# Kernel tuning notes

Hardware: AMD Instinct MI355X
Metric: run time of the kernel (lower is better)

## Reference

```python
import jax, jax.numpy as jnp
import numpy as np

KERNEL_SIZE = 37  # int((6*20-7)//3) = 37, already odd
PAD = (KERNEL_SIZE - 1) // 2  # 18


def moving_avg(x):
    """Edge-replicated moving average along token axis. x: [B, T, C]."""
    front = jnp.repeat(x[:, :1, :], PAD, axis=1)
    end = jnp.repeat(x[:, -1:, :], PAD, axis=1)
    xp = jnp.concatenate([front, x, end], axis=1)  # [B, T+2*PAD, C]
    cs = jnp.cumsum(xp, axis=1)
    cs = jnp.concatenate([jnp.zeros_like(cs[:, :1, :]), cs], axis=1)
    # window sums: length (T+2*PAD+1) - KERNEL_SIZE = T
    return (cs[:, KERNEL_SIZE:, :] - cs[:, :-KERNEL_SIZE, :]) / KERNEL_SIZE


def setup_inputs() -> dict:
    key = jax.random.key(0)
    ks = jax.random.split(key, 5)
    B, T, Cin, Cout = 4096, 17, 512, 512
    scale = 1.0 / np.sqrt(Cin)
    x = jax.random.normal(ks[0], (B, T, Cin), dtype=jnp.float32)
    W_seasonal = jax.random.uniform(ks[1], (T, Cout, Cin), jnp.float32, -scale, scale)
    b_seasonal = jax.random.uniform(ks[2], (T, Cout), jnp.float32, -scale, scale)
    W_trend = jax.random.uniform(ks[3], (T, Cout, Cin), jnp.float32, -scale, scale)
    b_trend = jax.random.uniform(ks[4], (T, Cout), jnp.float32, -scale, scale)
    return {"x": x, "W_seasonal": W_seasonal, "b_seasonal": b_seasonal,
            "W_trend": W_trend, "b_trend": b_trend}


def reference(x, W_seasonal, b_seasonal, W_trend, b_trend):
    trend = moving_avg(x)            # [B, T, Cin]
    seasonal = x - trend             # [B, T, Cin]
    # per-token (grouped) linear layers as one batched einsum
    s_out = jnp.einsum('btc,tdc->btd', seasonal, W_seasonal) + b_seasonal[None]
    t_out = jnp.einsum('btc,tdc->btd', trend, W_trend) + b_trend[None]
    return s_out + t_out
```

## Files before the change

kernel.cpp:

```cpp
#include <hip/hip_runtime.h>
#include <stdint.h>

#define B_N 4096
#define T_N 17
#define C_N 512

typedef __bf16 bf16x8 __attribute__((ext_vector_type(8)));
typedef float  f32x4  __attribute__((ext_vector_type(4)));

__device__ __forceinline__ unsigned short f2b(float f){
  unsigned u = __float_as_uint(f);
  return (unsigned short)((u + 0x7fffu + ((u >> 16) & 1u)) >> 16);
}
__device__ __forceinline__ unsigned pk2(float a, float b){
  return (unsigned)f2b(a) | ((unsigned)f2b(b) << 16);
}
__device__ __forceinline__ float blo(unsigned w){ return __uint_as_float(w << 16); }
__device__ __forceinline__ float bhi(unsigned w){ return __uint_as_float(w & 0xffff0000u); }

__device__ __forceinline__ void gll16(const void* g, void* l){
  __builtin_amdgcn_global_load_lds(
      (const __attribute__((address_space(1))) unsigned int*)g,
      (__attribute__((address_space(3))) unsigned int*)l, 16, 0, 0);
}

__global__ __launch_bounds__(256) void prep_w(
    const float* __restrict__ Ws, const float* __restrict__ Wt,
    unsigned short* __restrict__ wsb, unsigned short* __restrict__ dwb)
{
  const size_t i8 = ((size_t)blockIdx.x * 256 + threadIdx.x) * 8;
  float4 a0 = *(const float4*)(Ws + i8);
  float4 a1 = *(const float4*)(Ws + i8 + 4);
  float4 b0 = *(const float4*)(Wt + i8);
  float4 b1 = *(const float4*)(Wt + i8 + 4);
  uint4 oa, od;
  oa.x = pk2(a0.x, a0.y); oa.y = pk2(a0.z, a0.w);
  oa.z = pk2(a1.x, a1.y); oa.w = pk2(a1.z, a1.w);
  od.x = pk2(b0.x - a0.x, b0.y - a0.y); od.y = pk2(b0.z - a0.z, b0.w - a0.w);
  od.z = pk2(b1.x - a1.x, b1.y - a1.y); od.w = pk2(b1.z - a1.z, b1.w - a1.w);
  *(uint4*)(wsb + i8) = oa;
  *(uint4*)(dwb + i8) = od;
}

__global__ __launch_bounds__(256) void prep_bsum(
    const float* __restrict__ bs, const float* __restrict__ bt, float* __restrict__ o)
{
  const int i = blockIdx.x * 256 + threadIdx.x;
  o[i] = bs[i] + bt[i];
}

template<bool MAT>
__global__ __launch_bounds__(256) void prep_x(
    const float* __restrict__ x,
    unsigned short* __restrict__ o1,
    unsigned short* __restrict__ o2)
{
  const int idx = blockIdx.x * 256 + threadIdx.x;
  const int b = idx >> 6;
  const int c = (idx & 63) << 3;
  const float* xp = x + (size_t)b * (T_N * C_N) + c;
  float s[8] = {0,0,0,0,0,0,0,0};
  float f0[8], fl[8];
#pragma unroll
  for (int tt = 0; tt < T_N; ++tt){
    float4 w0 = *(const float4*)(xp + (size_t)tt * C_N);
    float4 w1 = *(const float4*)(xp + (size_t)tt * C_N + 4);
    float f[8] = {w0.x, w0.y, w0.z, w0.w, w1.x, w1.y, w1.z, w1.w};
    if (MAT){
      uint4 o;
      o.x = pk2(f[0],f[1]); o.y = pk2(f[2],f[3]);
      o.z = pk2(f[4],f[5]); o.w = pk2(f[6],f[7]);
      *(uint4*)(o1 + (size_t)b * (T_N*C_N) + (size_t)tt * C_N + c) = o;
    }
    if (tt == 0){
#pragma unroll
      for (int i=0;i<8;++i) f0[i] = f[i];
    }
    if (tt == T_N-1){
#pragma unroll
      for (int i=0;i<8;++i) fl[i] = f[i];
    }
#pragma unroll
    for (int i=0;i<8;++i) s[i] += f[i];
  }
  const float inv = 1.0f / 37.0f;
  float uu[8], vv[8];
#pragma unroll
  for (int i=0;i<8;++i){
    uu[i] = (s[i] + 18.0f * f0[i] + 2.0f * fl[i]) * inv;
    vv[i] = (fl[i] - f0[i]) * inv;
  }
  if (MAT){
#pragma unroll
    for (int tt = 0; tt < T_N; ++tt){
      const float tfv = (float)tt;
      float tr[8];
#pragma unroll
      for (int i=0;i<8;++i) tr[i] = fmaf(tfv, vv[i], uu[i]);
      uint4 o;
      o.x = pk2(tr[0],tr[1]); o.y = pk2(tr[2],tr[3]);
      o.z = pk2(tr[4],tr[5]); o.w = pk2(tr[6],tr[7]);
      *(uint4*)(o2 + (size_t)b * (T_N*C_N) + (size_t)tt * C_N + c) = o;
    }
  } else {
    uint4 ou, ov;
    ou.x = pk2(uu[0],uu[1]); ou.y = pk2(uu[2],uu[3]);
    ou.z = pk2(uu[4],uu[5]); ou.w = pk2(uu[6],uu[7]);
    ov.x = pk2(vv[0],vv[1]); ov.y = pk2(vv[2],vv[3]);
    ov.z = pk2(vv[4],vv[5]); ov.w = pk2(vv[6],vv[7]);
    *(uint4*)(o1 + (size_t)b * C_N + c) = ou;
    *(uint4*)(o2 + (size_t)b * C_N + c) = ov;
  }
}

template<bool MAT>
__global__ __launch_bounds__(256) void gemm_k(
    const float* __restrict__ x,
    const unsigned short* __restrict__ xb,
    const unsigned short* __restrict__ wsb,
    const unsigned short* __restrict__ dwb,
    const unsigned short* __restrict__ p1,
    const unsigned short* __restrict__ p2,
    const float* __restrict__ bsum,
    float* __restrict__ out)
{
  __shared__ alignas(16) unsigned short As[128*32];
  __shared__ alignas(16) unsigned short Bs[128*32];

  const int tid  = threadIdx.x;
  const int bx   = blockIdx.x;
  const int nt   = bx & 3;
  const int mt   = (bx >> 2) & 31;
  const int t    = bx >> 7;
  const int m0   = mt << 7;
  const int n0   = nt << 7;
  const int lane = tid & 63;
  const int wave = tid >> 6;
  const int wm   = (wave >> 1) << 6;
  const int wn   = (wave & 1) << 6;
  const int lr   = lane & 15;
  const int lj   = lane >> 4;
  const int swz  = (lr >> 1) & 3;

  f32x4 acc[4][4];
#pragma unroll
  for (int i=0;i<4;++i)
#pragma unroll
    for (int j=0;j<4;++j){ f32x4 z = {0.f,0.f,0.f,0.f}; acc[i][j] = z; }

  const float tf = (float)t;

  for (int kk = 0; kk < 32; ++kk){
    const int k0 = kk << 5;
    __syncthreads();
    if (MAT){
#pragma unroll
      for (int r = 0; r < 2; ++r){
        const int chunk = r*256 + tid;
        const int row = chunk >> 2;
        const int cgl = (chunk & 3) ^ ((row >> 1) & 3);
        const unsigned short* g = (k0 < 512)
          ? xb + ((size_t)(m0+row)*T_N + t)*C_N + k0 + cgl*8
          : p1 + ((size_t)(m0+row)*T_N + t)*C_N + (k0 - 512) + cgl*8;
        gll16(g, &As[chunk*8]);
      }
    } else if (k0 < 512){
#pragma unroll
      for (int r = 0; r < 2; ++r){
        const int chunk = r*256 + tid;
        const int row = chunk >> 2;
        const int cgl = (chunk & 3) ^ ((row >> 1) & 3);
        const float* g = x + ((size_t)(m0+row)*T_N + t)*C_N + k0 + cgl*8;
        float4 w0 = *(const float4*)g;
        float4 w1 = *(const float4*)(g + 4);
        uint4 o;
        o.x = pk2(w0.x, w0.y); o.y = pk2(w0.z, w0.w);
        o.z = pk2(w1.x, w1.y); o.w = pk2(w1.z, w1.w);
        *(uint4*)&As[chunk*8] = o;
      }
    } else {
#pragma unroll
      for (int r = 0; r < 2; ++r){
        const int chunk = r*256 + tid;
        const int row = chunk >> 2;
        const int cgl = (chunk & 3) ^ ((row >> 1) & 3);
        const size_t go = (size_t)(m0+row)*C_N + (k0 - 512) + cgl*8;
        uint4 uu = *(const uint4*)(p1 + go);
        uint4 vv = *(const uint4*)(p2 + go);
        uint4 o;
        o.x = pk2(fmaf(tf, blo(vv.x), blo(uu.x)), fmaf(tf, bhi(vv.x), bhi(uu.x)));
        o.y = pk2(fmaf(tf, blo(vv.y), blo(uu.y)), fmaf(tf, bhi(vv.y), bhi(uu.y)));
        o.z = pk2(fmaf(tf, blo(vv.z), blo(uu.z)), fmaf(tf, bhi(vv.z), bhi(uu.z)));
        o.w = pk2(fmaf(tf, blo(vv.w), blo(uu.w)), fmaf(tf, bhi(vv.w), bhi(uu.w)));
        *(uint4*)&As[chunk*8] = o;
      }
    }
#pragma unroll
    for (int r = 0; r < 2; ++r){
      const int chunk = r*256 + tid;
      const int row = chunk >> 2;
      const int cgl = (chunk & 3) ^ ((row >> 1) & 3);
      const unsigned short* g = (k0 < 512)
        ? wsb + ((size_t)t*C_N + n0 + row)*C_N + k0 + cgl*8
        : dwb + ((size_t)t*C_N + n0 + row)*C_N + (k0 - 512) + cgl*8;
      gll16(g, &Bs[chunk*8]);
    }
    __syncthreads();

    bf16x8 af[4], bf[4];
#pragma unroll
    for (int i=0;i<4;++i){
      const int row = wm + i*16 + lr;
      af[i] = *(const bf16x8*)&As[row*32 + ((lj ^ swz) * 8)];
    }
#pragma unroll
    for (int i=0;i<4;++i){
      const int row = wn + i*16 + lr;
      bf[i] = *(const bf16x8*)&Bs[row*32 + ((lj ^ swz) * 8)];
    }
#pragma unroll
    for (int mi=0;mi<4;++mi)
#pragma unroll
      for (int ni=0;ni<4;++ni)
        acc[mi][ni] = __builtin_amdgcn_mfma_f32_16x16x32_bf16(af[mi], bf[ni], acc[mi][ni], 0, 0, 0);
  }

  float bias[4];
#pragma unroll
  for (int ni=0;ni<4;++ni)
    bias[ni] = bsum[(size_t)t*C_N + n0 + wn + ni*16 + lr];

#pragma unroll
  for (int mi=0;mi<4;++mi){
#pragma unroll
    for (int r=0;r<4;++r){
      const int m = m0 + wm + mi*16 + lj*4 + r;
      float* op = out + ((size_t)m*T_N + t)*C_N + n0 + wn + lr;
#pragma unroll
      for (int ni=0;ni<4;++ni)
        op[ni*16] = acc[mi][ni][r] + bias[ni];
    }
  }
}

extern "C" void kernel_launch(void* const* d_in, const int* in_sizes, int n_in,
                              void* d_out, int out_size, void* d_ws, size_t ws_size,
                              hipStream_t stream)
{
  const float* x   = (const float*)d_in[0];
  const float* Wsl = (const float*)d_in[1];
  const float* bsl = (const float*)d_in[2];
  const float* Wtr = (const float*)d_in[3];
  const float* btr = (const float*)d_in[4];
  float* out = (float*)d_out;

  const size_t WSB_BYTES = (size_t)T_N*C_N*C_N*2;
  const size_t DW_BYTES  = WSB_BYTES;
  const size_t BS_BYTES  = (size_t)T_N*C_N*4;
  const size_t XB_BYTES  = (size_t)B_N*T_N*C_N*2;
  const size_t TR_BYTES  = XB_BYTES;
  const size_t UV_BYTES  = (size_t)B_N*C_N*2;

  char* ws = (char*)d_ws;
  unsigned short* wsb  = (unsigned short*)ws;
  unsigned short* dwb  = (unsigned short*)(ws + WSB_BYTES);
  float*          bsum = (float*)(ws + WSB_BYTES + DW_BYTES);
  char* rest = ws + WSB_BYTES + DW_BYTES + BS_BYTES;
  const bool mat = ws_size >= WSB_BYTES + DW_BYTES + BS_BYTES + XB_BYTES + TR_BYTES;

  prep_w<<<dim3(2176), dim3(256), 0, stream>>>(Wsl, Wtr, wsb, dwb);
  prep_bsum<<<dim3(34), dim3(256), 0, stream>>>(bsl, btr, bsum);
  if (mat){
    unsigned short* xb    = (unsigned short*)rest;
    unsigned short* trend = (unsigned short*)(rest + XB_BYTES);
    prep_x<true><<<dim3(1024), dim3(256), 0, stream>>>(x, xb, trend);
    gemm_k<true><<<dim3(2176), dim3(256), 0, stream>>>(x, xb, wsb, dwb, trend, nullptr, bsum, out);
  } else {
    unsigned short* u = (unsigned short*)rest;
    unsigned short* v = (unsigned short*)(rest + UV_BYTES);
    prep_x<false><<<dim3(1024), dim3(256), 0, stream>>>(x, u, v);
    gemm_k<false><<<dim3(2176), dim3(256), 0, stream>>>(x, nullptr, wsb, dwb, u, v, bsum, out);
  }
  (void)in_sizes; (void)n_in; (void)out_size;
}
```

Before: 416.7 us.

## Fuse prep kernels into one launch and compute trend from fp32 u/v in GEMM

Merges the weight conversion, bias sum and x preparation kernels into a single launch partitioned by block index, cutting launch count from four to two. The materialized path no longer writes a full bf16 trend tensor; the GEMM instead rebuilds trend rows from per-batch fp32 u/v vectors, which reduces prep writes and workspace size. The x-prep thread mapping also changes to split channels into two halves. The cost is more GEMM loads and math per trend K-tile, plus fp32 u/v reads of twice the bytes.

```diff
diff --git a/kernel.cpp b/kernel.cpp
--- a/kernel.cpp
+++ b/kernel.cpp
@@ -15,8 +15,6 @@
 __device__ __forceinline__ unsigned pk2(float a, float b){
   return (unsigned)f2b(a) | ((unsigned)f2b(b) << 16);
 }
-__device__ __forceinline__ float blo(unsigned w){ return __uint_as_float(w << 16); }
-__device__ __forceinline__ float bhi(unsigned w){ return __uint_as_float(w & 0xffff0000u); }
 
 __device__ __forceinline__ void gll16(const void* g, void* l){
   __builtin_amdgcn_global_load_lds(
@@ -24,92 +22,78 @@
       (__attribute__((address_space(3))) unsigned int*)l, 16, 0, 0);
 }
 
-__global__ __launch_bounds__(256) void prep_w(
+__global__ __launch_bounds__(256) void prep(
+    const float* __restrict__ x,
     const float* __restrict__ Ws, const float* __restrict__ Wt,
-    unsigned short* __restrict__ wsb, unsigned short* __restrict__ dwb)
+    const float* __restrict__ bs, const float* __restrict__ bt,
+    unsigned short* __restrict__ xb,
+    float* __restrict__ u, float* __restrict__ v,
+    unsigned short* __restrict__ wsb, unsigned short* __restrict__ dwb,
+    float* __restrict__ bsum, int mat)
 {
-  const size_t i8 = ((size_t)blockIdx.x * 256 + threadIdx.x) * 8;
-  float4 a0 = *(const float4*)(Ws + i8);
-  float4 a1 = *(const float4*)(Ws + i8 + 4);
-  float4 b0 = *(const float4*)(Wt + i8);
-  float4 b1 = *(const float4*)(Wt + i8 + 4);
-  uint4 oa, od;
-  oa.x = pk2(a0.x, a0.y); oa.y = pk2(a0.z, a0.w);
-  oa.z = pk2(a1.x, a1.y); oa.w = pk2(a1.z, a1.w);
-  od.x = pk2(b0.x - a0.x, b0.y - a0.y); od.y = pk2(b0.z - a0.z, b0.w - a0.w);
-  od.z = pk2(b1.x - a1.x, b1.y - a1.y); od.w = pk2(b1.z - a1.z, b1.w - a1.w);
-  *(uint4*)(wsb + i8) = oa;
-  *(uint4*)(dwb + i8) = od;
-}
-
-__global__ __launch_bounds__(256) void prep_bsum(
-    const float* __restrict__ bs, const float* __restrict__ bt, float* __restrict__ o)
-{
-  const int i = blockIdx.x * 256 + threadIdx.x;
-  o[i] = bs[i] + bt[i];
-}
-
-template<bool MAT>
-__global__ __launch_bounds__(256) void prep_x(
-    const float* __restrict__ x,
-    unsigned short* __restrict__ o1,
-    unsigned short* __restrict__ o2)
-{
-  const int idx = blockIdx.x * 256 + threadIdx.x;
-  const int b = idx >> 6;
-  const int c = (idx & 63) << 3;
-  const float* xp = x + (size_t)b * (T_N * C_N) + c;
-  float s[8] = {0,0,0,0,0,0,0,0};
-  float f0[8], fl[8];
-#pragma unroll
-  for (int tt = 0; tt < T_N; ++tt){
-    float4 w0 = *(const float4*)(xp + (size_t)tt * C_N);
-    float4 w1 = *(const float4*)(xp + (size_t)tt * C_N + 4);
-    float f[8] = {w0.x, w0.y, w0.z, w0.w, w1.x, w1.y, w1.z, w1.w};
-    if (MAT){
-      uint4 o;
-      o.x = pk2(f[0],f[1]); o.y = pk2(f[2],f[3]);
-      o.z = pk2(f[4],f[5]); o.w = pk2(f[6],f[7]);
-      *(uint4*)(o1 + (size_t)b * (T_N*C_N) + (size_t)tt * C_N + c) = o;
-    }
-    if (tt == 0){
-#pragma unroll
-      for (int i=0;i<8;++i) f0[i] = f[i];
-    }
-    if (tt == T_N-1){
-#pragma unroll
-      for (int i=0;i<8;++i) fl[i] = f[i];
-    }
-#pragma unroll
-    for (int i=0;i<8;++i) s[i] += f[i];
-  }
-  const float inv = 1.0f / 37.0f;
-  float uu[8], vv[8];
-#pragma unroll
-  for (int i=0;i<8;++i){
-    uu[i] = (s[i] + 18.0f * f0[i] + 2.0f * fl[i]) * inv;
-    vv[i] = (fl[i] - f0[i]) * inv;
-  }
-  if (MAT){
+  const int bid = blockIdx.x;
+  if (bid < 2176){
+    const size_t i8 = ((size_t)bid * 256 + threadIdx.x) * 8;
+    float4 a0 = *(const float4*)(Ws + i8);
+    float4 a1 = *(const float4*)(Ws + i8 + 4);
+    float4 b0 = *(const float4*)(Wt + i8);
+    float4 b1 = *(const float4*)(Wt + i8 + 4);
+    uint4 oa, od;
+    oa.x = pk2(a0.x, a0.y); oa.y = pk2(a0.z, a0.w);
+    oa.z = pk2(a1.x, a1.y); oa.w = pk2(a1.z, a1.w);
+    od.x = pk2(b0.x - a0.x, b0.y - a0.y); od.y = pk2(b0.z - a0.z, b0.w - a0.w);
+    od.z = pk2(b1.x - a1.x, b1.y - a1.y); od.w = pk2(b1.z - a1.z, b1.w - a1.w);
+    *(uint4*)(wsb + i8) = oa;
+    *(uint4*)(dwb + i8) = od;
+  } else if (bid < 2210){
+    const int i = (bid - 2176) * 256 + threadIdx.x;
+    if (i < T_N * C_N) bsum[i] = bs[i] + bt[i];
+  } else {
+    const int idx = (bid - 2210) * 256 + threadIdx.x;
+    const int b = idx >> 6;
+    const int l = idx & 63;
+    const int c0 = 4 * l;
+    const int c1 = 256 + 4 * l;
+    const float* xp = x + (size_t)b * (T_N * C_N);
+    float s[8] = {0,0,0,0,0,0,0,0};
+    float f0[8], fl[8];
 #pragma unroll
     for (int tt = 0; tt < T_N; ++tt){
-      const float tfv = (float)tt;
-      float tr[8];
-#pragma unroll
-      for (int i=0;i<8;++i) tr[i] = fmaf(tfv, vv[i], uu[i]);
-      uint4 o;
-      o.x = pk2(tr[0],tr[1]); o.y = pk2(tr[2],tr[3]);
-      o.z = pk2(tr[4],tr[5]); o.w = pk2(tr[6],tr[7]);
-      *(uint4*)(o2 + (size_t)b * (T_N*C_N) + (size_t)tt * C_N + c) = o;
-    }
-  } else {
-    uint4 ou, ov;
-    ou.x = pk2(uu[0],uu[1]); ou.y = pk2(uu[2],uu[3]);
-    ou.z = pk2(uu[4],uu[5]); ou.w = pk2(uu[6],uu[7]);
-    ov.x = pk2(vv[0],vv[1]); ov.y = pk2(vv[2],vv[3]);
-    ov.z = pk2(vv[4],vv[5]); ov.w = pk2(vv[6],vv[7]);
-    *(uint4*)(o1 + (size_t)b * C_N + c) = ou;
-    *(uint4*)(o2 + (size_t)b * C_N + c) = ov;
+      float4 w0 = *(const float4*)(xp + (size_t)tt * C_N + c0);
+      float4 w1 = *(const float4*)(xp + (size_t)tt * C_N + c1);
+      float f[8] = {w0.x, w0.y, w0.z, w0.w, w1.x, w1.y, w1.z, w1.w};
+      if (mat){
+        unsigned short* xo = xb + ((size_t)b * T_N + tt) * C_N;
+        uint2 p0, p1;
+        p0.x = pk2(f[0], f[1]); p0.y = pk2(f[2], f[3]);
+        p1.x = pk2(f[4], f[5]); p1.y = pk2(f[6], f[7]);
+        *(uint2*)(xo + c0) = p0;
+        *(uint2*)(xo + c1) = p1;
+      }
+      if (tt == 0){
+#pragma unroll
+        for (int i2=0;i2<8;++i2) f0[i2] = f[i2];
+      }
+      if (tt == T_N-1){
+#pragma unroll
+        for (int i2=0;i2<8;++i2) fl[i2] = f[i2];
+      }
+#pragma unroll
+      for (int i2=0;i2<8;++i2) s[i2] += f[i2];
+    }
+    const float inv = 1.0f / 37.0f;
+    float uu[8], vv[8];
+#pragma unroll
+    for (int i2=0;i2<8;++i2){
+      uu[i2] = (s[i2] + 18.0f * f0[i2] + 2.0f * fl[i2]) * inv;
+      vv[i2] = (fl[i2] - f0[i2]) * inv;
+    }
+    float* up = u + (size_t)b * C_N;
+    float* vp = v + (size_t)b * C_N;
+    *(float4*)(up + c0) = make_float4(uu[0], uu[1], uu[2], uu[3]);
+    *(float4*)(up + c1) = make_float4(uu[4], uu[5], uu[6], uu[7]);
+    *(float4*)(vp + c0) = make_float4(vv[0], vv[1], vv[2], vv[3]);
+    *(float4*)(vp + c1) = make_float4(vv[4], vv[5], vv[6], vv[7]);
   }
 }
 
@@ -119,8 +103,8 @@
     const unsigned short* __restrict__ xb,
     const unsigned short* __restrict__ wsb,
     const unsigned short* __restrict__ dwb,
-    const unsigned short* __restrict__ p1,
-    const unsigned short* __restrict__ p2,
+    const float* __restrict__ u,
+    const float* __restrict__ v,
     const float* __restrict__ bsum,
     float* __restrict__ out)
 {
@@ -153,30 +137,29 @@
   for (int kk = 0; kk < 32; ++kk){
     const int k0 = kk << 5;
     __syncthreads();
-    if (MAT){
-#pragma unroll
-      for (int r = 0; r < 2; ++r){
-        const int chunk = r*256 + tid;
-        const int row = chunk >> 2;
-        const int cgl = (chunk & 3) ^ ((row >> 1) & 3);
-        const unsigned short* g = (k0 < 512)
-          ? xb + ((size_t)(m0+row)*T_N + t)*C_N + k0 + cgl*8
-          : p1 + ((size_t)(m0+row)*T_N + t)*C_N + (k0 - 512) + cgl*8;
-        gll16(g, &As[chunk*8]);
-      }
-    } else if (k0 < 512){
-#pragma unroll
-      for (int r = 0; r < 2; ++r){
-        const int chunk = r*256 + tid;
-        const int row = chunk >> 2;
-        const int cgl = (chunk & 3) ^ ((row >> 1) & 3);
-        const float* g = x + ((size_t)(m0+row)*T_N + t)*C_N + k0 + cgl*8;
-        float4 w0 = *(const float4*)g;
-        float4 w1 = *(const float4*)(g + 4);
-        uint4 o;
-        o.x = pk2(w0.x, w0.y); o.y = pk2(w0.z, w0.w);
-        o.z = pk2(w1.x, w1.y); o.w = pk2(w1.z, w1.w);
-        *(uint4*)&As[chunk*8] = o;
+    if (k0 < 512){
+      if (MAT){
+#pragma unroll
+        for (int r = 0; r < 2; ++r){
+          const int chunk = r*256 + tid;
+          const int row = chunk >> 2;
+          const int cgl = (chunk & 3) ^ ((row >> 1) & 3);
+          gll16(xb + ((size_t)(m0+row)*T_N + t)*C_N + k0 + cgl*8, &As[chunk*8]);
+        }
+      } else {
+#pragma unroll
+        for (int r = 0; r < 2; ++r){
+          const int chunk = r*256 + tid;
+          const int row = chunk >> 2;
+          const int cgl = (chunk & 3) ^ ((row >> 1) & 3);
+          const float* g = x + ((size_t)(m0+row)*T_N + t)*C_N + k0 + cgl*8;
+          float4 w0 = *(const float4*)g;
+          float4 w1 = *(const float4*)(g + 4);
+          uint4 o;
+          o.x = pk2(w0.x, w0.y); o.y = pk2(w0.z, w0.w);
+          o.z = pk2(w1.x, w1.y); o.w = pk2(w1.z, w1.w);
+          *(uint4*)&As[chunk*8] = o;
+        }
       }
     } else {
 #pragma unroll
@@ -185,13 +168,15 @@
         const int row = chunk >> 2;
         const int cgl = (chunk & 3) ^ ((row >> 1) & 3);
         const size_t go = (size_t)(m0+row)*C_N + (k0 - 512) + cgl*8;
-        uint4 uu = *(const uint4*)(p1 + go);
-        uint4 vv = *(const uint4*)(p2 + go);
+        float4 u0 = *(const float4*)(u + go);
+        float4 u1 = *(const float4*)(u + go + 4);
+        float4 v0 = *(const float4*)(v + go);
+        float4 v1 = *(const float4*)(v + go + 4);
         uint4 o;
-        o.x = pk2(fmaf(tf, blo(vv.x), blo(uu.x)), fmaf(tf, bhi(vv.x), bhi(uu.x)));
-        o.y = pk2(fmaf(tf, blo(vv.y), blo(uu.y)), fmaf(tf, bhi(vv.y), bhi(uu.y)));
-        o.z = pk2(fmaf(tf, blo(vv.z), blo(uu.z)), fmaf(tf, bhi(vv.z), bhi(uu.z)));
-        o.w = pk2(fmaf(tf, blo(vv.w), blo(uu.w)), fmaf(tf, bhi(vv.w), bhi(uu.w)));
+        o.x = pk2(fmaf(tf, v0.x, u0.x), fmaf(tf, v0.y, u0.y));
+        o.y = pk2(fmaf(tf, v0.z, u0.z), fmaf(tf, v0.w, u0.w));
+        o.z = pk2(fmaf(tf, v1.x, u1.x), fmaf(tf, v1.y, u1.y));
+        o.w = pk2(fmaf(tf, v1.z, u1.z), fmaf(tf, v1.w, u1.w));
         *(uint4*)&As[chunk*8] = o;
       }
     }
@@ -257,29 +242,24 @@
   const size_t WSB_BYTES = (size_t)T_N*C_N*C_N*2;
   const size_t DW_BYTES  = WSB_BYTES;
   const size_t BS_BYTES  = (size_t)T_N*C_N*4;
+  const size_t U_BYTES   = (size_t)B_N*C_N*4;
+  const size_t V_BYTES   = U_BYTES;
   const size_t XB_BYTES  = (size_t)B_N*T_N*C_N*2;
-  const size_t TR_BYTES  = XB_BYTES;
-  const size_t UV_BYTES  = (size_t)B_N*C_N*2;
 
   char* ws = (char*)d_ws;
   unsigned short* wsb  = (unsigned short*)ws;
   unsigned short* dwb  = (unsigned short*)(ws + WSB_BYTES);
   float*          bsum = (float*)(ws + WSB_BYTES + DW_BYTES);
-  char* rest = ws + WSB_BYTES + DW_BYTES + BS_BYTES;
-  const bool mat = ws_size >= WSB_BYTES + DW_BYTES + BS_BYTES + XB_BYTES + TR_BYTES;
-
-  prep_w<<<dim3(2176), dim3(256), 0, stream>>>(Wsl, Wtr, wsb, dwb);
-  prep_bsum<<<dim3(34), dim3(256), 0, stream>>>(bsl, btr, bsum);
-  if (mat){
-    unsigned short* xb    = (unsigned short*)rest;
-    unsigned short* trend = (unsigned short*)(rest + XB_BYTES);
-    prep_x<true><<<dim3(1024), dim3(256), 0, stream>>>(x, xb, trend);
-    gemm_k<true><<<dim3(2176), dim3(256), 0, stream>>>(x, xb, wsb, dwb, trend, nullptr, bsum, out);
-  } else {
-    unsigned short* u = (unsigned short*)rest;
-    unsigned short* v = (unsigned short*)(rest + UV_BYTES);
-    prep_x<false><<<dim3(1024), dim3(256), 0, stream>>>(x, u, v);
+  float*          u    = (float*)(ws + WSB_BYTES + DW_BYTES + BS_BYTES);
+  float*          v    = (float*)(ws + WSB_BYTES + DW_BYTES + BS_BYTES + U_BYTES);
+  unsigned short* xb   = (unsigned short*)(ws + WSB_BYTES + DW_BYTES + BS_BYTES + U_BYTES + V_BYTES);
+  const bool mat = ws_size >= WSB_BYTES + DW_BYTES + BS_BYTES + U_BYTES + V_BYTES + XB_BYTES;
+
+  prep<<<dim3(3234), dim3(256), 0, stream>>>(x, Wsl, Wtr, bsl, btr,
+                                             xb, u, v, wsb, dwb, bsum, mat ? 1 : 0);
+  if (mat)
+    gemm_k<true><<<dim3(2176), dim3(256), 0, stream>>>(x, xb, wsb, dwb, u, v, bsum, out);
+  else
     gemm_k<false><<<dim3(2176), dim3(256), 0, stream>>>(x, nullptr, wsb, dwb, u, v, bsum, out);
-  }
   (void)in_sizes; (void)n_in; (void)out_size;
 }
```

Result: slower. 435.0 us (+4.4%).
